# Kernel tuning notes

Measured on AMD Instinct MI355X. Metric: run time of the kernel, lower is better.

## Reference

```python
import jax, jax.numpy as jnp
import numpy as np

N_NODES = 100000
N_EDGES = 1600000
IN_F, HID, N_CLS = 64, 128, 64


def setup_inputs() -> dict:
    key = jax.random.key(0)
    ks = jax.random.split(key, 7)
    return {
        "x": jax.random.normal(ks[0], (N_NODES, IN_F), dtype=jnp.float32),
        "W1": jax.random.normal(ks[1], (IN_F, HID), dtype=jnp.float32) * (1.0 / np.sqrt(IN_F)),
        "b1": jax.random.normal(ks[2], (HID,), dtype=jnp.float32) * 0.01,
        "W2": jax.random.normal(ks[3], (HID, N_CLS), dtype=jnp.float32) * (1.0 / np.sqrt(HID)),
        "b2": jax.random.normal(ks[4], (N_CLS,), dtype=jnp.float32) * 0.01,
        "src": jax.random.randint(ks[5], (N_EDGES,), 0, N_NODES, dtype=jnp.int32),
        "dst": jax.random.randint(ks[6], (N_EDGES,), 0, N_NODES, dtype=jnp.int32),
    }


def _gcn_layer(x, src, dst, W, b, n_nodes):
    # gather src features per edge, sum-scatter into dst nodes (SpMM), then linear
    agg = jax.ops.segment_sum(x[src], dst, num_segments=n_nodes)  # [N, d]
    return agg @ W + b


def reference(x, W1, b1, W2, b2, src, dst):
    n = x.shape[0]
    h = jax.nn.relu(_gcn_layer(x, src, dst, W1, b1, n))
    return _gcn_layer(h, src, dst, W2, b2, n)
```

## Files before the change

### kernel.cpp

```cpp
#include <hip/hip_runtime.h>

#define N_NODES 100000
#define N_EDGES 1600000
#define IN_F 64
#define HID 128
#define N_CLS 64

#define NPB2 512
#define NBK2 ((N_NODES + NPB2 - 1) / NPB2)
#define PAD 16
#define PCHUNK 8192
#define NPBLK ((N_EDGES + PCHUNK - 1) / PCHUNK)

__device__ __forceinline__ unsigned short f2bf(float f) {
    unsigned int u = __float_as_uint(f);
    u = (u + 0x7FFFu + ((u >> 16) & 1u)) >> 16;
    return (unsigned short)u;
}
__device__ __forceinline__ float bf2f(unsigned short h) {
    return __uint_as_float(((unsigned int)h) << 16);
}

__global__ void k_zero_f4(float4* __restrict__ p, int n4) {
    int i = blockIdx.x * blockDim.x + threadIdx.x;
    if (i < n4) p[i] = make_float4(0.f, 0.f, 0.f, 0.f);
}
__global__ void k_init_bias(float* __restrict__ out, const float* __restrict__ b2, int n) {
    int i = blockIdx.x * blockDim.x + threadIdx.x;
    if (i < n) out[i] = b2[i & 63];
}

__global__ void k_cvt(const float4* __restrict__ x4, uint4* __restrict__ xh, int n8) {
    int i = blockIdx.x * blockDim.x + threadIdx.x;
    if (i >= n8) return;
    float4 a = x4[2 * i], b = x4[2 * i + 1];
    uint4 o;
    o.x = (unsigned)f2bf(a.x) | ((unsigned)f2bf(a.y) << 16);
    o.y = (unsigned)f2bf(a.z) | ((unsigned)f2bf(a.w) << 16);
    o.z = (unsigned)f2bf(b.x) | ((unsigned)f2bf(b.y) << 16);
    o.w = (unsigned)f2bf(b.z) | ((unsigned)f2bf(b.w) << 16);
    xh[i] = o;
}

__global__ __launch_bounds__(256) void k_bhist(const int* __restrict__ dst,
                                               int* __restrict__ bcnt) {
    __shared__ int h[NBK2];
    for (int i = threadIdx.x; i < NBK2; i += 256) h[i] = 0;
    __syncthreads();
    int stride = gridDim.x * blockDim.x;
    for (int e = blockIdx.x * blockDim.x + threadIdx.x; e < N_EDGES; e += stride)
        atomicAdd(&h[dst[e] >> 9], 1);
    __syncthreads();
    for (int i = threadIdx.x; i < NBK2; i += 256) {
        int v = h[i];
        if (v) atomicAdd(&bcnt[i * PAD], v);
    }
}

__global__ __launch_bounds__(256) void k_bscan(const int* __restrict__ bcnt,
                                               int* __restrict__ boff,
                                               int* __restrict__ gcur) {
    __shared__ int s[NBK2];
    const int t = threadIdx.x;
    if (t < NBK2) s[t] = bcnt[t * PAD];
    __syncthreads();
    if (t == 0) {
        int run = 0;
        for (int i = 0; i < NBK2; ++i) { int v = s[i]; s[i] = run; run += v; }
    }
    __syncthreads();
    if (t < NBK2) { boff[t] = s[t]; gcur[t * PAD] = s[t]; }
    if (t == 0) boff[NBK2] = N_EDGES;
}

__global__ __launch_bounds__(256) void k_part(const int* __restrict__ src,
                                              const int* __restrict__ dst,
                                              int* __restrict__ gcur,
                                              int* __restrict__ eb) {
    __shared__ int hist[NBK2];
    __shared__ int gbase[NBK2];
    __shared__ int lcur[NBK2];
    const int t = threadIdx.x;
    const int e0 = blockIdx.x * PCHUNK;
    int e1 = e0 + PCHUNK; if (e1 > N_EDGES) e1 = N_EDGES;
    for (int i = t; i < NBK2; i += 256) hist[i] = 0;
    __syncthreads();
    for (int e = e0 + t; e < e1; e += 256) atomicAdd(&hist[dst[e] >> 9], 1);
    __syncthreads();
    if (t < NBK2) {
        int c = hist[t];
        gbase[t] = c ? atomicAdd(&gcur[t * PAD], c) : 0;
        lcur[t] = 0;
    }
    __syncthreads();
    for (int e = e0 + t; e < e1; e += 256) {
        int d = dst[e];
        int b = d >> 9;
        int r = atomicAdd(&lcur[b], 1);
        eb[gbase[b] + r] = ((d & 511) << 17) | src[e];
    }
}

__global__ __launch_bounds__(512) void k_fill3(const int* __restrict__ eb,
                                               const int* __restrict__ boff,
                                               int* __restrict__ off,
                                               int* __restrict__ es) {
    __shared__ int ldeg[NPB2];
    __shared__ int sc[2][NPB2];
    const int t = threadIdx.x;
    const int b = blockIdx.x;
    const int bbase = boff[b], bend = boff[b + 1];

    ldeg[t] = 0;
    __syncthreads();
    for (int i = bbase + t; i < bend; i += 512) atomicAdd(&ldeg[eb[i] >> 17], 1);
    __syncthreads();

    int v = ldeg[t];
    sc[0][t] = v;
    __syncthreads();
    int cur = 0;
    for (int d = 1; d < NPB2; d <<= 1) {
        int x = sc[cur][t];
        if (t >= d) x += sc[cur][t - d];
        sc[cur ^ 1][t] = x;
        __syncthreads();
        cur ^= 1;
    }
    int ex = sc[cur][t] - v;

    const int n0 = b * NPB2;
    if (n0 + t < N_NODES) off[n0 + t] = bbase + ex;
    if (b == NBK2 - 1 && t == 0) off[N_NODES] = N_EDGES;

    ldeg[t] = ex;
    __syncthreads();

    for (int i = bbase + t; i < bend; i += 512) {
        int p = eb[i];
        int r = atomicAdd(&ldeg[p >> 17], 1);
        es[bbase + r] = p & 0x1FFFF;
    }
}

__global__ __launch_bounds__(256) void k_gather2(const unsigned* __restrict__ feat,
                                                 const int* __restrict__ es,
                                                 const int* __restrict__ off,
                                                 const float* __restrict__ bias,
                                                 float* __restrict__ out) {
    const int wave = threadIdx.x >> 6;
    const int lane = threadIdx.x & 63;
    const int half = lane >> 5;
    const int l32 = lane & 31;
    const int n = blockIdx.x * 8 + wave * 2 + half;
    const int beg = off[n], end = off[n + 1];
    const int hb = half << 5;
    float acc0 = 0.f, acc1 = 0.f;
    for (int base = beg; base < end; base += 32) {
        int m = end - base; if (m > 32) m = 32;
        int id = (l32 < m) ? es[base + l32] : 0;
        int k = 0;
        for (; k + 4 <= m; k += 4) {
            int s0 = __shfl(id, hb | (k + 0));
            int s1 = __shfl(id, hb | (k + 1));
            int s2 = __shfl(id, hb | (k + 2));
            int s3 = __shfl(id, hb | (k + 3));
            unsigned u0 = feat[(unsigned)s0 * 32u + l32];
            unsigned u1 = feat[(unsigned)s1 * 32u + l32];
            unsigned u2 = feat[(unsigned)s2 * 32u + l32];
            unsigned u3 = feat[(unsigned)s3 * 32u + l32];
            acc0 += (__uint_as_float(u0 << 16) + __uint_as_float(u1 << 16))
                  + (__uint_as_float(u2 << 16) + __uint_as_float(u3 << 16));
            acc1 += (__uint_as_float(u0 & 0xFFFF0000u) + __uint_as_float(u1 & 0xFFFF0000u))
                  + (__uint_as_float(u2 & 0xFFFF0000u) + __uint_as_float(u3 & 0xFFFF0000u));
        }
        for (; k < m; ++k) {
            int s = __shfl(id, hb | k);
            unsigned u = feat[(unsigned)s * 32u + l32];
            acc0 += __uint_as_float(u << 16);
            acc1 += __uint_as_float(u & 0xFFFF0000u);
        }
    }
    if (bias) { acc0 += bias[l32 * 2]; acc1 += bias[l32 * 2 + 1]; }
    float2 o; o.x = acc0; o.y = acc1;
    *(float2*)&out[(size_t)n * 64 + l32 * 2] = o;
}

__global__ __launch_bounds__(256) void k_gatherF(const float* __restrict__ feat,
                                                 const int* __restrict__ es,
                                                 const int* __restrict__ off,
                                                 const float* __restrict__ bias,
                                                 float* __restrict__ out) {
    const int wave = threadIdx.x >> 6;
    const int lane = threadIdx.x & 63;
    const int n = blockIdx.x * 4 + wave;
    if (n >= N_NODES) return;
    const int beg = off[n], end = off[n + 1];
    float acc = bias ? bias[lane] : 0.f;
    for (int base = beg; base < end; base += 64) {
        int m = end - base; if (m > 64) m = 64;
        int id = (lane < m) ? es[base + lane] : 0;
        int k = 0;
        for (; k + 4 <= m; k += 4) {
            int s0 = __shfl(id, k), s1 = __shfl(id, k + 1);
            int s2 = __shfl(id, k + 2), s3 = __shfl(id, k + 3);
            float v0 = feat[(size_t)s0 * 64 + lane];
            float v1 = feat[(size_t)s1 * 64 + lane];
            float v2 = feat[(size_t)s2 * 64 + lane];
            float v3 = feat[(size_t)s3 * 64 + lane];
            acc += (v0 + v1) + (v2 + v3);
        }
        for (; k < m; ++k) {
            int s = __shfl(id, k);
            acc += feat[(size_t)s * 64 + lane];
        }
    }
    out[(size_t)n * 64 + lane] = acc;
}

__global__ void k_scatter64(const float* __restrict__ feat,
                            const int* __restrict__ src,
                            const int* __restrict__ dst,
                            float* __restrict__ out) {
    int i = blockIdx.x * blockDim.x + threadIdx.x;
    int e = i >> 4;
    if (e >= N_EDGES) return;
    int j = (i & 15) << 2;
    int s = src[e];
    int d = dst[e];
    float4 v = *reinterpret_cast<const float4*>(feat + (size_t)s * 64 + j);
    float* o = out + (size_t)d * 64 + j;
    atomicAdd(o + 0, v.x);
    atomicAdd(o + 1, v.y);
    atomicAdd(o + 2, v.z);
    atomicAdd(o + 3, v.w);
}

#define MROWS 32
#define XS_S 68
#define HS2_S 152

__device__ __forceinline__ void fma4(float4& a, float s, const float4& wv) {
    a.x = fmaf(s, wv.x, a.x);
    a.y = fmaf(s, wv.y, a.y);
    a.z = fmaf(s, wv.z, a.z);
    a.w = fmaf(s, wv.w, a.w);
}

__global__ __launch_bounds__(256, 3) void k_gemm1(const float* __restrict__ A,
                                                  unsigned short* __restrict__ H,
                                                  const float* __restrict__ W1,
                                                  const float* __restrict__ b1) {
    __shared__ float Ws[64 * 128];
    __shared__ float xs[MROWS * XS_S];
    __shared__ float b1s[128];
    const int t = threadIdx.x;
    const int row0 = blockIdx.x * MROWS;

    {
        const float4* w4 = (const float4*)W1;
        float4* s4 = (float4*)Ws;
        for (int i = t; i < 2048; i += 256) s4[i] = w4[i];
    }
    if (t < 128) b1s[t] = b1[t];
#pragma unroll
    for (int c = 0; c < 2; ++c) {
        int lin = t + c * 256;
        int r = lin >> 4, k4 = lin & 15;
        float4 v = *(const float4*)(A + (size_t)(row0 + r) * 64 + k4 * 4);
        *(float4*)&xs[r * XS_S + k4 * 4] = v;
    }
    __syncthreads();

    const int rg = t >> 5, cg = t & 31;
    const int r0 = rg * 4, c0 = cg * 4;
    float4 bv = *(const float4*)&b1s[c0];
    float4 acc0 = bv, acc1 = bv, acc2 = bv, acc3 = bv;
#pragma unroll 4
    for (int k4 = 0; k4 < 16; ++k4) {
        float4 a0 = *(const float4*)&xs[(r0 + 0) * XS_S + k4 * 4];
        float4 a1 = *(const float4*)&xs[(r0 + 1) * XS_S + k4 * 4];
        float4 a2 = *(const float4*)&xs[(r0 + 2) * XS_S + k4 * 4];
        float4 a3 = *(const float4*)&xs[(r0 + 3) * XS_S + k4 * 4];
        float4 w0 = *(const float4*)&Ws[(k4 * 4 + 0) * 128 + c0];
        float4 w1 = *(const float4*)&Ws[(k4 * 4 + 1) * 128 + c0];
        float4 w2 = *(const float4*)&Ws[(k4 * 4 + 2) * 128 + c0];
        float4 w3 = *(const float4*)&Ws[(k4 * 4 + 3) * 128 + c0];
        fma4(acc0, a0.x, w0); fma4(acc0, a0.y, w1); fma4(acc0, a0.z, w2); fma4(acc0, a0.w, w3);
        fma4(acc1, a1.x, w0); fma4(acc1, a1.y, w1); fma4(acc1, a1.z, w2); fma4(acc1, a1.w, w3);
        fma4(acc2, a2.x, w0); fma4(acc2, a2.y, w1); fma4(acc2, a2.z, w2); fma4(acc2, a2.w, w3);
        fma4(acc3, a3.x, w0); fma4(acc3, a3.y, w1); fma4(acc3, a3.z, w2); fma4(acc3, a3.w, w3);
    }
    ushort4 o;
    o.x = f2bf(fmaxf(acc0.x, 0.f)); o.y = f2bf(fmaxf(acc0.y, 0.f));
    o.z = f2bf(fmaxf(acc0.z, 0.f)); o.w = f2bf(fmaxf(acc0.w, 0.f));
    *(ushort4*)&H[(size_t)(row0 + r0 + 0) * 128 + c0] = o;
    o.x = f2bf(fmaxf(acc1.x, 0.f)); o.y = f2bf(fmaxf(acc1.y, 0.f));
    o.z = f2bf(fmaxf(acc1.z, 0.f)); o.w = f2bf(fmaxf(acc1.w, 0.f));
    *(ushort4*)&H[(size_t)(row0 + r0 + 1) * 128 + c0] = o;
    o.x = f2bf(fmaxf(acc2.x, 0.f)); o.y = f2bf(fmaxf(acc2.y, 0.f));
    o.z = f2bf(fmaxf(acc2.z, 0.f)); o.w = f2bf(fmaxf(acc2.w, 0.f));
    *(ushort4*)&H[(size_t)(row0 + r0 + 2) * 128 + c0] = o;
    o.x = f2bf(fmaxf(acc3.x, 0.f)); o.y = f2bf(fmaxf(acc3.y, 0.f));
    o.z = f2bf(fmaxf(acc3.z, 0.f)); o.w = f2bf(fmaxf(acc3.w, 0.f));
    *(ushort4*)&H[(size_t)(row0 + r0 + 3) * 128 + c0] = o;
}

__global__ __launch_bounds__(256, 3) void k_gemm2(const unsigned short* __restrict__ H,
                                                  unsigned short* __restrict__ zh,
                                                  const float* __restrict__ W2) {
    __shared__ float Ws[128 * 64];
    __shared__ unsigned short hsb[MROWS * HS2_S];
    const int t = threadIdx.x;
    const int row0 = blockIdx.x * MROWS;

    {
        const float4* w4 = (const float4*)W2;
        float4* s4 = (float4*)Ws;
        for (int i = t; i < 2048; i += 256) s4[i] = w4[i];
    }
#pragma unroll
    for (int c = 0; c < 2; ++c) {
        int lin = t + c * 256;
        int r = lin >> 4, k8 = lin & 15;
        uint4 v = *(const uint4*)(H + (size_t)(row0 + r) * 128 + k8 * 8);
        *(uint4*)&hsb[r * HS2_S + k8 * 8] = v;
    }
    __syncthreads();

    const int rg = t >> 4, cg = t & 15;
    const int r0 = rg * 2, c0 = cg * 4;
    float4 acc0 = make_float4(0.f, 0.f, 0.f, 0.f);
    float4 acc1 = make_float4(0.f, 0.f, 0.f, 0.f);
#pragma unroll 4
    for (int k4 = 0; k4 < 32; ++k4) {
        ushort4 u0 = *(const ushort4*)&hsb[(r0 + 0) * HS2_S + k4 * 4];
        ushort4 u1 = *(const ushort4*)&hsb[(r0 + 1) * HS2_S + k4 * 4];
        float4 w0 = *(const float4*)&Ws[(k4 * 4 + 0) * 64 + c0];
        float4 w1 = *(const float4*)&Ws[(k4 * 4 + 1) * 64 + c0];
        float4 w2 = *(const float4*)&Ws[(k4 * 4 + 2) * 64 + c0];
        float4 w3 = *(const float4*)&Ws[(k4 * 4 + 3) * 64 + c0];
        fma4(acc0, bf2f(u0.x), w0); fma4(acc0, bf2f(u0.y), w1);
        fma4(acc0, bf2f(u0.z), w2); fma4(acc0, bf2f(u0.w), w3);
        fma4(acc1, bf2f(u1.x), w0); fma4(acc1, bf2f(u1.y), w1);
        fma4(acc1, bf2f(u1.z), w2); fma4(acc1, bf2f(u1.w), w3);
    }
    ushort4 o0, o1;
    o0.x = f2bf(acc0.x); o0.y = f2bf(acc0.y); o0.z = f2bf(acc0.z); o0.w = f2bf(acc0.w);
    o1.x = f2bf(acc1.x); o1.y = f2bf(acc1.y); o1.z = f2bf(acc1.z); o1.w = f2bf(acc1.w);
    *(ushort4*)&zh[(size_t)(row0 + r0 + 0) * 64 + c0] = o0;
    *(ushort4*)&zh[(size_t)(row0 + r0 + 1) * 64 + c0] = o1;
}

__global__ __launch_bounds__(256, 2) void k_mlpF(float* __restrict__ A,
                                                 const float* __restrict__ W1,
                                                 const float* __restrict__ b1,
                                                 const float* __restrict__ W2) {
    __shared__ float Ws[64 * 128];
    __shared__ float xs[MROWS * XS_S];
    __shared__ float hs[MROWS * 132];
    __shared__ float b1s[128];
    const int t = threadIdx.x;
    const int row0 = blockIdx.x * MROWS;

    {
        const float4* w4 = (const float4*)W1;
        float4* s4 = (float4*)Ws;
        for (int i = t; i < 2048; i += 256) s4[i] = w4[i];
    }
    if (t < 128) b1s[t] = b1[t];
#pragma unroll
    for (int c = 0; c < 2; ++c) {
        int lin = t + c * 256;
        int r = lin >> 4, k4 = lin & 15;
        float4 v = *(const float4*)(A + (size_t)(row0 + r) * 64 + k4 * 4);
        *(float4*)&xs[r * XS_S + k4 * 4] = v;
    }
    __syncthreads();
    {
        const int rg = t >> 5, cg = t & 31;
        const int r0 = rg * 4, c0 = cg * 4;
        float4 bv = *(const float4*)&b1s[c0];
        float4 acc0 = bv, acc1 = bv, acc2 = bv, acc3 = bv;
#pragma unroll 4
        for (int k4 = 0; k4 < 16; ++k4) {
            float4 a0 = *(const float4*)&xs[(r0 + 0) * XS_S + k4 * 4];
            float4 a1 = *(const float4*)&xs[(r0 + 1) * XS_S + k4 * 4];
            float4 a2 = *(const float4*)&xs[(r0 + 2) * XS_S + k4 * 4];
            float4 a3 = *(const float4*)&xs[(r0 + 3) * XS_S + k4 * 4];
            float4 w0 = *(const float4*)&Ws[(k4 * 4 + 0) * 128 + c0];
            float4 w1 = *(const float4*)&Ws[(k4 * 4 + 1) * 128 + c0];
            float4 w2 = *(const float4*)&Ws[(k4 * 4 + 2) * 128 + c0];
            float4 w3 = *(const float4*)&Ws[(k4 * 4 + 3) * 128 + c0];
            fma4(acc0, a0.x, w0); fma4(acc0, a0.y, w1); fma4(acc0, a0.z, w2); fma4(acc0, a0.w, w3);
            fma4(acc1, a1.x, w0); fma4(acc1, a1.y, w1); fma4(acc1, a1.z, w2); fma4(acc1, a1.w, w3);
            fma4(acc2, a2.x, w0); fma4(acc2, a2.y, w1); fma4(acc2, a2.z, w2); fma4(acc2, a2.w, w3);
            fma4(acc3, a3.x, w0); fma4(acc3, a3.y, w1); fma4(acc3, a3.z, w2); fma4(acc3, a3.w, w3);
        }
        float4 h;
        h.x = fmaxf(acc0.x, 0.f); h.y = fmaxf(acc0.y, 0.f); h.z = fmaxf(acc0.z, 0.f); h.w = fmaxf(acc0.w, 0.f);
        *(float4*)&hs[(r0 + 0) * 132 + c0] = h;
        h.x = fmaxf(acc1.x, 0.f); h.y = fmaxf(acc1.y, 0.f); h.z = fmaxf(acc1.z, 0.f); h.w = fmaxf(acc1.w, 0.f);
        *(float4*)&hs[(r0 + 1) * 132 + c0] = h;
        h.x = fmaxf(acc2.x, 0.f); h.y = fmaxf(acc2.y, 0.f); h.z = fmaxf(acc2.z, 0.f); h.w = fmaxf(acc2.w, 0.f);
        *(float4*)&hs[(r0 + 2) * 132 + c0] = h;
        h.x = fmaxf(acc3.x, 0.f); h.y = fmaxf(acc3.y, 0.f); h.z = fmaxf(acc3.z, 0.f); h.w = fmaxf(acc3.w, 0.f);
        *(float4*)&hs[(r0 + 3) * 132 + c0] = h;
    }
    __syncthreads();
    {
        const float4* w4 = (const float4*)W2;
        float4* s4 = (float4*)Ws;
        for (int i = t; i < 2048; i += 256) s4[i] = w4[i];
    }
    __syncthreads();
    {
        const int rg = t >> 4, cg = t & 15;
        const int r0 = rg * 2, c0 = cg * 4;
        float4 acc0 = make_float4(0.f, 0.f, 0.f, 0.f);
        float4 acc1 = make_float4(0.f, 0.f, 0.f, 0.f);
#pragma unroll 4
        for (int k4 = 0; k4 < 32; ++k4) {
            float4 h0 = *(const float4*)&hs[(r0 + 0) * 132 + k4 * 4];
            float4 h1 = *(const float4*)&hs[(r0 + 1) * 132 + k4 * 4];
            float4 w0 = *(const float4*)&Ws[(k4 * 4 + 0) * 64 + c0];
            float4 w1 = *(const float4*)&Ws[(k4 * 4 + 1) * 64 + c0];
            float4 w2 = *(const float4*)&Ws[(k4 * 4 + 2) * 64 + c0];
            float4 w3 = *(const float4*)&Ws[(k4 * 4 + 3) * 64 + c0];
            fma4(acc0, h0.x, w0); fma4(acc0, h0.y, w1); fma4(acc0, h0.z, w2); fma4(acc0, h0.w, w3);
            fma4(acc1, h1.x, w0); fma4(acc1, h1.y, w1); fma4(acc1, h1.z, w2); fma4(acc1, h1.w, w3);
        }
        *(float4*)(A + (size_t)(row0 + r0 + 0) * 64 + c0) = acc0;
        *(float4*)(A + (size_t)(row0 + r0 + 1) * 64 + c0) = acc1;
    }
}

static inline size_t alignup(size_t v, size_t a) { return (v + a - 1) & ~(a - 1); }

extern "C" void kernel_launch(void* const* d_in, const int* in_sizes, int n_in,
                              void* d_out, int out_size, void* d_ws, size_t ws_size,
                              hipStream_t stream) {
    const float* x  = (const float*)d_in[0];
    const float* W1 = (const float*)d_in[1];
    const float* b1 = (const float*)d_in[2];
    const float* W2 = (const float*)d_in[3];
    const float* b2 = (const float*)d_in[4];
    const int* src  = (const int*)d_in[5];
    const int* dst  = (const int*)d_in[6];
    float* out = (float*)d_out;

    const int nfeat = N_NODES * 64;
    const int nfeat4 = nfeat / 4;

    char* base = (char*)d_ws;
    size_t o = 0;
    size_t o_xh   = o;                  o = alignup(o + (size_t)nfeat * 2, 64);
    size_t o_es   = o;                  o = alignup(o + (size_t)N_EDGES * 4, 64);
    size_t o_off  = o;                  o = alignup(o + (size_t)(N_NODES + 1) * 4, 64);
    size_t o_bcnt = o;                  o = alignup(o + (size_t)NBK2 * PAD * 4, 64);
    size_t o_gcur = o;                  o = alignup(o + (size_t)NBK2 * PAD * 4, 64);
    size_t o_boff = o;                  o = alignup(o + (size_t)(NBK2 + 1) * 4, 64);
    size_t o_shrd = o;                  o = alignup(o + (size_t)nfeat * 4, 64);
    size_t need1 = o;

    unsigned short* xh = (unsigned short*)(base + o_xh);
    int* es    = (int*)(base + o_es);
    int* off   = (int*)(base + o_off);
    int* bcnt  = (int*)(base + o_bcnt);
    int* gcur  = (int*)(base + o_gcur);
    int* boff  = (int*)(base + o_boff);
    int* eb    = (int*)(base + o_shrd);
    float* A   = (float*)(base + o_shrd);
    unsigned short* H = (unsigned short*)(base + o_shrd);
    unsigned short* zh = xh;

    size_t p = 0;
    size_t p_A    = p;   p = alignup(p + (size_t)nfeat * 4, 64);
    size_t p_eb   = p;   p = alignup(p + (size_t)N_EDGES * 4, 64);
    size_t p_es   = p;   p = alignup(p + (size_t)N_EDGES * 4, 64);
    size_t p_off  = p;   p = alignup(p + (size_t)(N_NODES + 1) * 4, 64);
    size_t p_bcnt = p;   p = alignup(p + (size_t)NBK2 * PAD * 4, 64);
    size_t p_gcur = p;   p = alignup(p + (size_t)NBK2 * PAD * 4, 64);
    size_t p_boff = p;   p = alignup(p + (size_t)(NBK2 + 1) * 4, 64);
    size_t need2 = p;

    if (ws_size >= need1) {
        k_cvt<<<(nfeat / 8 + 255) / 256, 256, 0, stream>>>((const float4*)x, (uint4*)xh, nfeat / 8);
        hipMemsetAsync(bcnt, 0, (size_t)NBK2 * PAD * 4, stream);
        k_bhist<<<512, 256, 0, stream>>>(dst, bcnt);
        k_bscan<<<1, 256, 0, stream>>>(bcnt, boff, gcur);
        k_part<<<NPBLK, 256, 0, stream>>>(src, dst, gcur, eb);
        k_fill3<<<NBK2, 512, 0, stream>>>(eb, boff, off, es);

        k_gather2<<<N_NODES / 8, 256, 0, stream>>>((const unsigned*)xh, es, off, nullptr, A);
        k_gemm1<<<N_NODES / MROWS, 256, 0, stream>>>(A, H, W1, b1);
        k_gemm2<<<N_NODES / MROWS, 256, 0, stream>>>(H, zh, W2);
        k_gather2<<<N_NODES / 8, 256, 0, stream>>>((const unsigned*)zh, es, off, b2, out);
    } else if (ws_size >= need2) {
        float* A2  = (float*)(base + p_A);
        int* eb2   = (int*)(base + p_eb);
        int* es2   = (int*)(base + p_es);
        int* off2  = (int*)(base + p_off);
        int* bcnt2 = (int*)(base + p_bcnt);
        int* gcur2 = (int*)(base + p_gcur);
        int* boff2 = (int*)(base + p_boff);

        hipMemsetAsync(bcnt2, 0, (size_t)NBK2 * PAD * 4, stream);
        k_bhist<<<512, 256, 0, stream>>>(dst, bcnt2);
        k_bscan<<<1, 256, 0, stream>>>(bcnt2, boff2, gcur2);
        k_part<<<NPBLK, 256, 0, stream>>>(src, dst, gcur2, eb2);
        k_fill3<<<NBK2, 512, 0, stream>>>(eb2, boff2, off2, es2);

        k_gatherF<<<(N_NODES + 3) / 4, 256, 0, stream>>>(x, es2, off2, nullptr, A2);
        k_mlpF<<<N_NODES / MROWS, 256, 0, stream>>>(A2, W1, b1, W2);
        k_gatherF<<<(N_NODES + 3) / 4, 256, 0, stream>>>(A2, es2, off2, b2, out);
    } else {
        float* A3 = (float*)d_ws;
        k_zero_f4<<<(nfeat4 + 255) / 256, 256, 0, stream>>>((float4*)A3, nfeat4);
        int threads = N_EDGES * 16;
        k_scatter64<<<(threads + 255) / 256, 256, 0, stream>>>(x, src, dst, A3);
        k_mlpF<<<N_NODES / MROWS, 256, 0, stream>>>(A3, W1, b1, W2);
        k_init_bias<<<(nfeat + 255) / 256, 256, 0, stream>>>(out, b2, nfeat);
        k_scatter64<<<(threads + 255) / 256, 256, 0, stream>>>(A3, src, dst, out);
    }
}
```

Baseline: 205.6 us.

## Replace atomic bucket partition with deterministic per-block count and column scan

The CSR build no longer uses a global histogram plus global atomic cursors. It now has each of 512 edge chunks write its own per-bucket counts into a matrix, scans each bucket column to get per-chunk offsets, and scans the bucket totals. The scatter pass then places edges without global atomics. Buckets shrink from 512 to 256 nodes, so the fill kernel runs 256-thread blocks. The intermediate fallback path is removed, and the change adds two more small launches plus a count matrix in the workspace.

```diff
diff --git a/kernel.cpp b/kernel.cpp
--- a/kernel.cpp
+++ b/kernel.cpp
@@ -6,11 +6,10 @@
 #define HID 128
 #define N_CLS 64
 
-#define NPB2 512
+#define NPB2 256
 #define NBK2 ((N_NODES + NPB2 - 1) / NPB2)
-#define PAD 16
-#define PCHUNK 8192
-#define NPBLK ((N_EDGES + PCHUNK - 1) / PCHUNK)
+#define NPBLK 512
+#define PCHUNK (N_EDGES / NPBLK)
 
 __device__ __forceinline__ unsigned short f2bf(float f) {
     unsigned int u = __float_as_uint(f);
@@ -42,66 +41,82 @@
     xh[i] = o;
 }
 
-__global__ __launch_bounds__(256) void k_bhist(const int* __restrict__ dst,
-                                               int* __restrict__ bcnt) {
+__global__ __launch_bounds__(256) void k_count(const int* __restrict__ dst,
+                                               int* __restrict__ C) {
     __shared__ int h[NBK2];
-    for (int i = threadIdx.x; i < NBK2; i += 256) h[i] = 0;
-    __syncthreads();
-    int stride = gridDim.x * blockDim.x;
-    for (int e = blockIdx.x * blockDim.x + threadIdx.x; e < N_EDGES; e += stride)
-        atomicAdd(&h[dst[e] >> 9], 1);
-    __syncthreads();
-    for (int i = threadIdx.x; i < NBK2; i += 256) {
-        int v = h[i];
-        if (v) atomicAdd(&bcnt[i * PAD], v);
-    }
-}
-
-__global__ __launch_bounds__(256) void k_bscan(const int* __restrict__ bcnt,
-                                               int* __restrict__ boff,
-                                               int* __restrict__ gcur) {
-    __shared__ int s[NBK2];
-    const int t = threadIdx.x;
-    if (t < NBK2) s[t] = bcnt[t * PAD];
-    __syncthreads();
-    if (t == 0) {
-        int run = 0;
-        for (int i = 0; i < NBK2; ++i) { int v = s[i]; s[i] = run; run += v; }
-    }
-    __syncthreads();
-    if (t < NBK2) { boff[t] = s[t]; gcur[t * PAD] = s[t]; }
+    const int t = threadIdx.x;
+    for (int i = t; i < NBK2; i += 256) h[i] = 0;
+    __syncthreads();
+    const int e0 = blockIdx.x * PCHUNK;
+    int e1 = e0 + PCHUNK; if (e1 > N_EDGES) e1 = N_EDGES;
+    for (int e = e0 + t; e < e1; e += 256) atomicAdd(&h[dst[e] >> 8], 1);
+    __syncthreads();
+    for (int i = t; i < NBK2; i += 256) C[blockIdx.x * NBK2 + i] = h[i];
+}
+
+__global__ __launch_bounds__(NPBLK) void k_colscan(int* __restrict__ C,
+                                                   int* __restrict__ btot) {
+    __shared__ int sc[2][NPBLK];
+    const int t = threadIdx.x;
+    const int bucket = blockIdx.x;
+    int v = C[t * NBK2 + bucket];
+    sc[0][t] = v;
+    __syncthreads();
+    int cur = 0;
+    for (int d = 1; d < NPBLK; d <<= 1) {
+        int x = sc[cur][t];
+        if (t >= d) x += sc[cur][t - d];
+        sc[cur ^ 1][t] = x;
+        __syncthreads();
+        cur ^= 1;
+    }
+    C[t * NBK2 + bucket] = sc[cur][t] - v;
+    if (t == NPBLK - 1) btot[bucket] = sc[cur][t];
+}
+
+__global__ __launch_bounds__(512) void k_btscan(const int* __restrict__ btot,
+                                                int* __restrict__ boff) {
+    __shared__ int sc[2][512];
+    const int t = threadIdx.x;
+    int v = (t < NBK2) ? btot[t] : 0;
+    sc[0][t] = v;
+    __syncthreads();
+    int cur = 0;
+    for (int d = 1; d < 512; d <<= 1) {
+        int x = sc[cur][t];
+        if (t >= d) x += sc[cur][t - d];
+        sc[cur ^ 1][t] = x;
+        __syncthreads();
+        cur ^= 1;
+    }
+    if (t < NBK2) boff[t] = sc[cur][t] - v;
     if (t == 0) boff[NBK2] = N_EDGES;
 }
 
-__global__ __launch_bounds__(256) void k_part(const int* __restrict__ src,
+__global__ __launch_bounds__(256) void k_scat(const int* __restrict__ src,
                                               const int* __restrict__ dst,
-                                              int* __restrict__ gcur,
+                                              const int* __restrict__ C,
+                                              const int* __restrict__ boff,
                                               int* __restrict__ eb) {
-    __shared__ int hist[NBK2];
     __shared__ int gbase[NBK2];
     __shared__ int lcur[NBK2];
     const int t = threadIdx.x;
+    for (int i = t; i < NBK2; i += 256) {
+        gbase[i] = boff[i] + C[blockIdx.x * NBK2 + i];
+        lcur[i] = 0;
+    }
+    __syncthreads();
     const int e0 = blockIdx.x * PCHUNK;
     int e1 = e0 + PCHUNK; if (e1 > N_EDGES) e1 = N_EDGES;
-    for (int i = t; i < NBK2; i += 256) hist[i] = 0;
-    __syncthreads();
-    for (int e = e0 + t; e < e1; e += 256) atomicAdd(&hist[dst[e] >> 9], 1);
-    __syncthreads();
-    if (t < NBK2) {
-        int c = hist[t];
-        gbase[t] = c ? atomicAdd(&gcur[t * PAD], c) : 0;
-        lcur[t] = 0;
-    }
-    __syncthreads();
     for (int e = e0 + t; e < e1; e += 256) {
         int d = dst[e];
-        int b = d >> 9;
+        int b = d >> 8;
         int r = atomicAdd(&lcur[b], 1);
-        eb[gbase[b] + r] = ((d & 511) << 17) | src[e];
-    }
-}
-
-__global__ __launch_bounds__(512) void k_fill3(const int* __restrict__ eb,
+        eb[gbase[b] + r] = ((d & 255) << 17) | src[e];
+    }
+}
+
+__global__ __launch_bounds__(256) void k_fill3(const int* __restrict__ eb,
                                                const int* __restrict__ boff,
                                                int* __restrict__ off,
                                                int* __restrict__ es) {
@@ -113,7 +128,7 @@
 
     ldeg[t] = 0;
     __syncthreads();
-    for (int i = bbase + t; i < bend; i += 512) atomicAdd(&ldeg[eb[i] >> 17], 1);
+    for (int i = bbase + t; i < bend; i += 256) atomicAdd(&ldeg[eb[i] >> 17], 1);
     __syncthreads();
 
     int v = ldeg[t];
@@ -136,7 +151,7 @@
     ldeg[t] = ex;
     __syncthreads();
 
-    for (int i = bbase + t; i < bend; i += 512) {
+    for (int i = bbase + t; i < bend; i += 256) {
         int p = eb[i];
         int r = atomicAdd(&ldeg[p >> 17], 1);
         es[bbase + r] = p & 0x1FFFF;
@@ -186,38 +201,6 @@
     *(float2*)&out[(size_t)n * 64 + l32 * 2] = o;
 }
 
-__global__ __launch_bounds__(256) void k_gatherF(const float* __restrict__ feat,
-                                                 const int* __restrict__ es,
-                                                 const int* __restrict__ off,
-                                                 const float* __restrict__ bias,
-                                                 float* __restrict__ out) {
-    const int wave = threadIdx.x >> 6;
-    const int lane = threadIdx.x & 63;
-    const int n = blockIdx.x * 4 + wave;
-    if (n >= N_NODES) return;
-    const int beg = off[n], end = off[n + 1];
-    float acc = bias ? bias[lane] : 0.f;
-    for (int base = beg; base < end; base += 64) {
-        int m = end - base; if (m > 64) m = 64;
-        int id = (lane < m) ? es[base + lane] : 0;
-        int k = 0;
-        for (; k + 4 <= m; k += 4) {
-            int s0 = __shfl(id, k), s1 = __shfl(id, k + 1);
-            int s2 = __shfl(id, k + 2), s3 = __shfl(id, k + 3);
-            float v0 = feat[(size_t)s0 * 64 + lane];
-            float v1 = feat[(size_t)s1 * 64 + lane];
-            float v2 = feat[(size_t)s2 * 64 + lane];
-            float v3 = feat[(size_t)s3 * 64 + lane];
-            acc += (v0 + v1) + (v2 + v3);
-        }
-        for (; k < m; ++k) {
-            int s = __shfl(id, k);
-            acc += feat[(size_t)s * 64 + lane];
-        }
-    }
-    out[(size_t)n * 64 + lane] = acc;
-}
-
 __global__ void k_scatter64(const float* __restrict__ feat,
                             const int* __restrict__ src,
                             const int* __restrict__ dst,
@@ -454,66 +437,38 @@
 
     char* base = (char*)d_ws;
     size_t o = 0;
-    size_t o_xh   = o;                  o = alignup(o + (size_t)nfeat * 2, 64);
-    size_t o_es   = o;                  o = alignup(o + (size_t)N_EDGES * 4, 64);
-    size_t o_off  = o;                  o = alignup(o + (size_t)(N_NODES + 1) * 4, 64);
-    size_t o_bcnt = o;                  o = alignup(o + (size_t)NBK2 * PAD * 4, 64);
-    size_t o_gcur = o;                  o = alignup(o + (size_t)NBK2 * PAD * 4, 64);
-    size_t o_boff = o;                  o = alignup(o + (size_t)(NBK2 + 1) * 4, 64);
-    size_t o_shrd = o;                  o = alignup(o + (size_t)nfeat * 4, 64);
+    size_t o_xh   = o;   o = alignup(o + (size_t)nfeat * 2, 64);
+    size_t o_es   = o;   o = alignup(o + (size_t)N_EDGES * 4, 64);
+    size_t o_off  = o;   o = alignup(o + (size_t)(N_NODES + 1) * 4, 64);
+    size_t o_C    = o;   o = alignup(o + (size_t)NPBLK * NBK2 * 4, 64);
+    size_t o_btot = o;   o = alignup(o + (size_t)NBK2 * 4, 64);
+    size_t o_boff = o;   o = alignup(o + (size_t)(NBK2 + 1) * 4, 64);
+    size_t o_shrd = o;   o = alignup(o + (size_t)nfeat * 4, 64);
     size_t need1 = o;
 
     unsigned short* xh = (unsigned short*)(base + o_xh);
     int* es    = (int*)(base + o_es);
     int* off   = (int*)(base + o_off);
-    int* bcnt  = (int*)(base + o_bcnt);
-    int* gcur  = (int*)(base + o_gcur);
+    int* C     = (int*)(base + o_C);
+    int* btot  = (int*)(base + o_btot);
     int* boff  = (int*)(base + o_boff);
     int* eb    = (int*)(base + o_shrd);
     float* A   = (float*)(base + o_shrd);
     unsigned short* H = (unsigned short*)(base + o_shrd);
     unsigned short* zh = xh;
 
-    size_t p = 0;
-    size_t p_A    = p;   p = alignup(p + (size_t)nfeat * 4, 64);
-    size_t p_eb   = p;   p = alignup(p + (size_t)N_EDGES * 4, 64);
-    size_t p_es   = p;   p = alignup(p + (size_t)N_EDGES * 4, 64);
-    size_t p_off  = p;   p = alignup(p + (size_t)(N_NODES + 1) * 4, 64);
-    size_t p_bcnt = p;   p = alignup(p + (size_t)NBK2 * PAD * 4, 64);
-    size_t p_gcur = p;   p = alignup(p + (size_t)NBK2 * PAD * 4, 64);
-    size_t p_boff = p;   p = alignup(p + (size_t)(NBK2 + 1) * 4, 64);
-    size_t need2 = p;
-
     if (ws_size >= need1) {
         k_cvt<<<(nfeat / 8 + 255) / 256, 256, 0, stream>>>((const float4*)x, (uint4*)xh, nfeat / 8);
-        hipMemsetAsync(bcnt, 0, (size_t)NBK2 * PAD * 4, stream);
-        k_bhist<<<512, 256, 0, stream>>>(dst, bcnt);
-        k_bscan<<<1, 256, 0, stream>>>(bcnt, boff, gcur);
-        k_part<<<NPBLK, 256, 0, stream>>>(src, dst, gcur, eb);
-        k_fill3<<<NBK2, 512, 0, stream>>>(eb, boff, off, es);
+        k_count<<<NPBLK, 256, 0, stream>>>(dst, C);
+        k_colscan<<<NBK2, NPBLK, 0, stream>>>(C, btot);
+        k_btscan<<<1, 512, 0, stream>>>(btot, boff);
+        k_scat<<<NPBLK, 256, 0, stream>>>(src, dst, C, boff, eb);
+        k_fill3<<<NBK2, 256, 0, stream>>>(eb, boff, off, es);
 
         k_gather2<<<N_NODES / 8, 256, 0, stream>>>((const unsigned*)xh, es, off, nullptr, A);
         k_gemm1<<<N_NODES / MROWS, 256, 0, stream>>>(A, H, W1, b1);
         k_gemm2<<<N_NODES / MROWS, 256, 0, stream>>>(H, zh, W2);
         k_gather2<<<N_NODES / 8, 256, 0, stream>>>((const unsigned*)zh, es, off, b2, out);
-    } else if (ws_size >= need2) {
-        float* A2  = (float*)(base + p_A);
-        int* eb2   = (int*)(base + p_eb);
-        int* es2   = (int*)(base + p_es);
-        int* off2  = (int*)(base + p_off);
-        int* bcnt2 = (int*)(base + p_bcnt);
-        int* gcur2 = (int*)(base + p_gcur);
-        int* boff2 = (int*)(base + p_boff);
-
-        hipMemsetAsync(bcnt2, 0, (size_t)NBK2 * PAD * 4, stream);
-        k_bhist<<<512, 256, 0, stream>>>(dst, bcnt2);
-        k_bscan<<<1, 256, 0, stream>>>(bcnt2, boff2, gcur2);
-        k_part<<<NPBLK, 256, 0, stream>>>(src, dst, gcur2, eb2);
-        k_fill3<<<NBK2, 512, 0, stream>>>(eb2, boff2, off2, es2);
-
-        k_gatherF<<<(N_NODES + 3) / 4, 256, 0, stream>>>(x, es2, off2, nullptr, A2);
-        k_mlpF<<<N_NODES / MROWS, 256, 0, stream>>>(A2, W1, b1, W2);
-        k_gatherF<<<(N_NODES + 3) / 4, 256, 0, stream>>>(A2, es2, off2, b2, out);
     } else {
         float* A3 = (float*)d_ws;
         k_zero_f4<<<(nfeat4 + 255) / 256, 256, 0, stream>>>((float4*)A3, nfeat4);
```

Measured after the change: 184.6 us. 10.2% less time.
